# Kernel tuning notes

Measured on AMD Instinct MI355X. Metric: run time of the kernel, lower is better.

The kernel has to match this reference:

```python
import jax, jax.numpy as jnp
import numpy as np

K = 3  # kernel_size

def setup_inputs() -> dict:
    key = jax.random.key(0)
    k1, k2, k3 = jax.random.split(key, 3)
    B, T, G, F, O = 4, 512, 129, 96, 96
    x = jax.random.normal(k1, (B, T, G, F), dtype=jnp.float32)
    # kaiming_uniform_(a=sqrt(5)) -> bound = sqrt(6/((1+5)*fan_in)) = 1/sqrt(fan_in), fan_in = F*K
    fan_in = F * K
    wb = 1.0 / np.sqrt(fan_in)
    weight = jax.random.uniform(k2, (G, O, F, K), dtype=jnp.float32, minval=-wb, maxval=wb)
    bias = jax.random.uniform(k3, (G, O), dtype=jnp.float32, minval=-wb, maxval=wb)
    return {"x": x, "weight": weight, "bias": bias}

def reference(x, weight, bias):
    # x: [B, T, G, F]; weight: [G, O, F, K]; bias: [G, O]
    B, T, G, F = x.shape
    pad = K // 2
    xp = jnp.pad(x, ((0, 0), (pad, pad), (0, 0), (0, 0)))  # [B, T+2p, G, F]
    # gather K shifted views -> [B, T, G, F, K] (same windows as unfold with padding K//2)
    xw = jnp.stack([xp[:, k:k + T] for k in range(K)], axis=-1)
    out = jnp.einsum('btgfk,gofk->btgo', xw, weight)
    out = out + bias  # broadcast [G, O] over [B, T, G, O]
    return out
```

## Files before the change

kernel.cpp:

```cpp
#include <hip/hip_runtime.h>
#include <hip/hip_bf16.h>

typedef unsigned short ushort_t;
typedef __attribute__((ext_vector_type(8))) short short8;
typedef __attribute__((ext_vector_type(4))) float floatx4;

#define G_   129
#define F_   96
#define O_   96
#define T_   512
#define KD   288
#define LDB  296
#define SROW 40
#define SLAB (36 * SROW)

__device__ __forceinline__ unsigned f2bf(float f) {
    unsigned u = __builtin_bit_cast(unsigned, f);
    u += 0x7FFFu + ((u >> 16) & 1u);
    return u >> 16;
}
__device__ __forceinline__ unsigned pk2(float a, float b) {
    return f2bf(a) | (f2bf(b) << 16);
}

__global__ void wt_permute(const float* __restrict__ w, ushort_t* __restrict__ wt) {
    int i = blockIdx.x * 256 + threadIdx.x;
    const int total = G_ * O_ * KD;
    if (i >= total) return;
    int base = i / KD;
    int kd = i - base * KD;
    int kk = kd / F_;
    int f  = kd - kk * F_;
    wt[i] = (ushort_t)f2bf(w[base * KD + f * 3 + kk]);
}

__global__ __launch_bounds__(512, 4) void conv_mfma(
    const float* __restrict__ x, const ushort_t* __restrict__ wt,
    const float* __restrict__ bias, float* __restrict__ out)
{
    __shared__ __align__(16) ushort_t Wl[O_ * LDB];
    __shared__ __align__(16) ushort_t Xs[8 * SLAB];

    const int g    = blockIdx.y;
    const int m0   = blockIdx.x * 256;
    const int tid  = threadIdx.x;
    const int wave = tid >> 6;
    const int lane = tid & 63;
    const int ln   = lane & 15;
    const int q    = lane >> 4;

    {
        const ushort_t* src = wt + (size_t)g * (O_ * KD);
        for (int idx = tid; idx < O_ * 36; idx += 512) {
            int o = idx / 36;
            int s = idx - o * 36;
            *(short8*)&Wl[o * LDB + s * 8] = *(const short8*)&src[o * KD + s * 8];
        }
    }
    __syncthreads();

    const int m0r = m0 + wave * 32;
    const int b   = m0r >> 9;
    const int tb  = m0r & 511;

    const float* tp[5];
    int  laddr[5];
    bool wr[5], vld[5];
    #pragma unroll
    for (int i = 0; i < 5; ++i) {
        int task = i * 64 + lane;
        int row = task >> 3;
        int seg = task & 7;
        int tl = tb + row - 1;
        wr[i]  = row < 34;
        vld[i] = wr[i] && ((unsigned)tl < (unsigned)T_);
        int tc = tl < 0 ? 0 : (tl > T_ - 1 ? T_ - 1 : tl);
        tp[i] = x + ((size_t)((b * T_ + tc) * G_ + g) * F_ + seg * 4);
        laddr[i] = wave * SLAB + row * SROW + seg * 4;
    }

    auto issueX = [&](int fb, floatx4* v) {
        #pragma unroll
        for (int i = 0; i < 5; ++i)
            v[i] = *(const floatx4*)(tp[i] + fb * 32);
    };
    auto writeX = [&](const floatx4* v) {
        #pragma unroll
        for (int i = 0; i < 5; ++i) {
            if (wr[i]) {
                unsigned lo = pk2(v[i][0], v[i][1]);
                unsigned hi = pk2(v[i][2], v[i][3]);
                if (!vld[i]) { lo = 0u; hi = 0u; }
                uint2 d; d.x = lo; d.y = hi;
                *(uint2*)&Xs[laddr[i]] = d;
            }
        }
    };

    floatx4 acc[2][6];
    #pragma unroll
    for (int s = 0; s < 2; ++s)
        #pragma unroll
        for (int nt = 0; nt < 6; ++nt)
            acc[s][nt] = (floatx4){0.f, 0.f, 0.f, 0.f};

    floatx4 cur[5], nxt[5];
    issueX(0, cur);

    #pragma unroll
    for (int fb = 0; fb < 3; ++fb) {
        if (fb < 2) issueX(fb + 1, nxt);
        writeX(cur);

        #pragma unroll
        for (int kk = 0; kk < 3; ++kk) {
            const short8 a0 = *(const short8*)&Xs[wave * SLAB + (ln + kk) * SROW + q * 8];
            const short8 a1 = *(const short8*)&Xs[wave * SLAB + (16 + ln + kk) * SROW + q * 8];
            const int c32 = (kk * 3 + fb) * 32;
            #pragma unroll
            for (int nt = 0; nt < 6; ++nt) {
                const short8 bb = *(const short8*)&Wl[(nt * 16 + ln) * LDB + c32 + q * 8];
                acc[0][nt] = __builtin_amdgcn_mfma_f32_16x16x32_bf16(a0, bb, acc[0][nt], 0, 0, 0);
                acc[1][nt] = __builtin_amdgcn_mfma_f32_16x16x32_bf16(a1, bb, acc[1][nt], 0, 0, 0);
            }
        }
        #pragma unroll
        for (int i = 0; i < 5; ++i) cur[i] = nxt[i];
    }

    #pragma unroll
    for (int s = 0; s < 2; ++s) {
        int mbase = m0 + wave * 32 + s * 16 + q * 4;
        #pragma unroll
        for (int nt = 0; nt < 6; ++nt) {
            int o = nt * 16 + ln;
            float bv = bias[g * O_ + o];
            #pragma unroll
            for (int r = 0; r < 4; ++r) {
                int m = mbase + r;
                out[(size_t)(m * G_ + g) * O_ + o] = acc[s][nt][r] + bv;
            }
        }
    }
}

extern "C" void kernel_launch(void* const* d_in, const int* in_sizes, int n_in,
                              void* d_out, int out_size, void* d_ws, size_t ws_size,
                              hipStream_t stream) {
    const float* x    = (const float*)d_in[0];
    const float* w    = (const float*)d_in[1];
    const float* bias = (const float*)d_in[2];
    float* out = (float*)d_out;
    ushort_t* wt = (ushort_t*)d_ws;

    const int total_w = G_ * O_ * KD;
    wt_permute<<<dim3((total_w + 255) / 256), dim3(256), 0, stream>>>(w, wt);

    dim3 grid(2048 / 256, G_);
    conv_mfma<<<grid, dim3(512), 0, stream>>>(x, wt, bias, out);
}
```

Before: 218.5 us.

## Fuse weight permute and bf16 conversion into conv kernel, drop prep launch

Removes the separate weight-permutation kernel. Each conv block now reads its group's fp32 weights directly, converts them to bf16, and scatters them into the shared-memory layout. The first X load is issued before the weight staging so the two overlap. This saves a kernel launch and a workspace round trip. In exchange, each of the 8 blocks per group re-reads and re-converts fp32 weights (twice the bytes of bf16) and does scalar 2-byte LDS scatter stores.

```diff
diff --git a/kernel.cpp b/kernel.cpp
--- a/kernel.cpp
+++ b/kernel.cpp
@@ -13,6 +13,7 @@
 #define LDB  296
 #define SROW 40
 #define SLAB (36 * SROW)
+#define WCHUNKS 6912
 
 __device__ __forceinline__ unsigned f2bf(float f) {
     unsigned u = __builtin_bit_cast(unsigned, f);
@@ -23,19 +24,8 @@
     return f2bf(a) | (f2bf(b) << 16);
 }
 
-__global__ void wt_permute(const float* __restrict__ w, ushort_t* __restrict__ wt) {
-    int i = blockIdx.x * 256 + threadIdx.x;
-    const int total = G_ * O_ * KD;
-    if (i >= total) return;
-    int base = i / KD;
-    int kd = i - base * KD;
-    int kk = kd / F_;
-    int f  = kd - kk * F_;
-    wt[i] = (ushort_t)f2bf(w[base * KD + f * 3 + kk]);
-}
-
 __global__ __launch_bounds__(512, 4) void conv_mfma(
-    const float* __restrict__ x, const ushort_t* __restrict__ wt,
+    const float* __restrict__ x, const float* __restrict__ w,
     const float* __restrict__ bias, float* __restrict__ out)
 {
     __shared__ __align__(16) ushort_t Wl[O_ * LDB];
@@ -48,16 +38,6 @@
     const int lane = tid & 63;
     const int ln   = lane & 15;
     const int q    = lane >> 4;
-
-    {
-        const ushort_t* src = wt + (size_t)g * (O_ * KD);
-        for (int idx = tid; idx < O_ * 36; idx += 512) {
-            int o = idx / 36;
-            int s = idx - o * 36;
-            *(short8*)&Wl[o * LDB + s * 8] = *(const short8*)&src[o * KD + s * 8];
-        }
-    }
-    __syncthreads();
 
     const int m0r = m0 + wave * 32;
     const int b   = m0r >> 9;
@@ -97,15 +77,45 @@
         }
     };
 
+    floatx4 cur[5], nxt[5];
+    issueX(0, cur);
+
+    {
+        const float* wg = w + (size_t)g * (O_ * KD);
+        #pragma unroll
+        for (int bb = 0; bb < 2; ++bb) {
+            floatx4 wv[7];
+            #pragma unroll
+            for (int i = 0; i < 7; ++i) {
+                int chunk = (bb * 7 + i) * 512 + tid;
+                int ch = chunk < WCHUNKS ? chunk : WCHUNKS - 1;
+                wv[i] = *(const floatx4*)(wg + (size_t)ch * 4);
+            }
+            #pragma unroll
+            for (int i = 0; i < 7; ++i) {
+                int chunk = (bb * 7 + i) * 512 + tid;
+                if (chunk < WCHUNKS) {
+                    int o   = chunk / 72;
+                    int rem = (chunk - o * 72) * 4;
+                    #pragma unroll
+                    for (int e = 0; e < 4; ++e) {
+                        int re = rem + e;
+                        int f  = re / 3;
+                        int kk = re - f * 3;
+                        Wl[o * LDB + kk * 96 + f] = (ushort_t)f2bf(wv[i][e]);
+                    }
+                }
+            }
+        }
+    }
+    __syncthreads();
+
     floatx4 acc[2][6];
     #pragma unroll
     for (int s = 0; s < 2; ++s)
         #pragma unroll
         for (int nt = 0; nt < 6; ++nt)
             acc[s][nt] = (floatx4){0.f, 0.f, 0.f, 0.f};
-
-    floatx4 cur[5], nxt[5];
-    issueX(0, cur);
 
     #pragma unroll
     for (int fb = 0; fb < 3; ++fb) {
@@ -151,11 +161,7 @@
     const float* w    = (const float*)d_in[1];
     const float* bias = (const float*)d_in[2];
     float* out = (float*)d_out;
-    ushort_t* wt = (ushort_t*)d_ws;
-
-    const int total_w = G_ * O_ * KD;
-    wt_permute<<<dim3((total_w + 255) / 256), dim3(256), 0, stream>>>(w, wt);
 
     dim3 grid(2048 / 256, G_);
-    conv_mfma<<<grid, dim3(512), 0, stream>>>(x, wt, bias, out);
+    conv_mfma<<<grid, dim3(512), 0, stream>>>(x, w, bias, out);
 }
```

Result: no change. 222.5 us (+1.8%).
